# Performance work log

Hardware: AMD Instinct MI355X
Metric: run time of the kernel (lower is better)

Reference implementation:

```python
import jax, jax.numpy as jnp
import numpy as np

N = 2_000_000
C = 128
B = 50_000


def setup_inputs() -> dict:
    key = jax.random.key(0)
    k1, k2, k3 = jax.random.split(key, 3)
    x = jax.random.normal(k1, (N, C), dtype=jnp.float32)
    weight_c = jax.random.normal(k2, (C, C), dtype=jnp.float32) * (1.0 / np.sqrt(C))
    batch = jnp.sort(jax.random.randint(k3, (N,), 0, B, dtype=jnp.int64))
    return {"x": x, "weight_c": weight_c, "batch": batch, "num_segments": B}


def reference(x, weight_c, batch, num_segments):
    # global_mean_pool: segment sum / count (count clamped to >=1)
    sums = jax.ops.segment_sum(x, batch, num_segments=num_segments)          # [B, C]
    ones = jnp.ones((x.shape[0], 1), dtype=x.dtype)
    counts = jax.ops.segment_sum(ones, batch, num_segments=num_segments)    # [B, 1]
    c = sums / jnp.maximum(counts, 1.0)
    # context transform
    c = jnp.tanh(c @ weight_c)                                              # [B, C]
    # gather context back to nodes
    c_nodes = c[batch]                                                      # [N, C]
    # sigmoid gate on per-node dot product, then global_add_pool
    gate = jax.nn.sigmoid(jnp.sum(x * c_nodes, axis=1, keepdims=True))      # [N, 1]
    h = jax.ops.segment_sum(gate * x, batch, num_segments=num_segments)     # [B, C]
    return h
```

## Files before the change

### kernel.cpp

```cpp
#include <hip/hip_runtime.h>
#include <math.h>

#define C        128
#define BLK      256
#define WPB      (BLK / 64)
#define MAXSLOT  12
#define NROW     (4 * MAXSLOT)
#define WSTRIDE  68

__device__ __forceinline__ float4 f4add(float4 a, float4 b) {
    float4 r; r.x = a.x + b.x; r.y = a.y + b.y; r.z = a.z + b.z; r.w = a.w + b.w; return r;
}
__device__ __forceinline__ float4 f4shfl_xor(float4 v, int m) {
    float4 r;
    r.x = __shfl_xor(v.x, m, 64);
    r.y = __shfl_xor(v.y, m, 64);
    r.z = __shfl_xor(v.z, m, 64);
    r.w = __shfl_xor(v.w, m, 64);
    return r;
}
__device__ __forceinline__ float fast_tanh(float v) {
    const float t = __expf(2.0f * v);
    return 1.0f - 2.0f / (t + 1.0f);
}
__device__ __forceinline__ float fast_sigmoid(float v) {
    return 1.0f / (1.0f + __expf(-v));
}
__device__ __forceinline__ uint32_t pack2(float a, float b) {
    uint32_t ua = __float_as_uint(a), ub = __float_as_uint(b);
    ua = (ua + 0x7FFFu + ((ua >> 16) & 1u)) >> 16;
    ub = (ub + 0x7FFFu + ((ub >> 16) & 1u)) & 0xFFFF0000u;
    return ua | ub;
}
__device__ __forceinline__ float4 unpack4(uint32_t a, uint32_t b) {
    float4 v;
    v.x = __uint_as_float(a << 16);
    v.y = __uint_as_float(a & 0xFFFF0000u);
    v.z = __uint_as_float(b << 16);
    v.w = __uint_as_float(b & 0xFFFF0000u);
    return v;
}
__device__ __forceinline__ float row16_sum(float d) {
    d += __int_as_float(__builtin_amdgcn_update_dpp(0, __float_as_int(d), 0x128, 0xF, 0xF, true));
    d += __int_as_float(__builtin_amdgcn_update_dpp(0, __float_as_int(d), 0x124, 0xF, 0xF, true));
    d += __int_as_float(__builtin_amdgcn_update_dpp(0, __float_as_int(d), 0x122, 0xF, 0xF, true));
    d += __int_as_float(__builtin_amdgcn_update_dpp(0, __float_as_int(d), 0x121, 0xF, 0xF, true));
    return d;
}
__device__ __forceinline__ float dot8(float4 lo, float4 hi, float4 clo, float4 chi) {
    float a = lo.x * clo.x + lo.y * clo.y;
    float b = lo.z * clo.z + lo.w * clo.w;
    float c = hi.x * chi.x + hi.y * chi.y;
    float d = hi.z * chi.z + hi.w * chi.w;
    return (a + b) + (c + d);
}

extern "C" __global__ __launch_bounds__(BLK)
__attribute__((amdgpu_waves_per_eu(2, 2)))
void cba_pipe_reg_kernel(const float* __restrict__ x,
                         const float* __restrict__ W,
                         const int* __restrict__ batch,
                         float* __restrict__ out,
                         int N, int B, int totalWaves)
{
    __shared__ uint32_t sWb[C * WSTRIDE];
    __shared__ float4   sMean[WPB * 32];

    const int t    = threadIdx.x;
    const int lane = t & 63;
    const int wid  = t >> 6;
    const int rg   = lane >> 4;
    const int c16  = lane & 15;

    const float2* W2 = (const float2*)W;
    for (int p = t; p < C * 64; p += BLK) {
        const int k = p >> 6, j = p & 63;
        const float2 wv = W2[p];
        sWb[k * WSTRIDE + ((j + ((k >> 5) << 3)) & 63)] = pack2(wv.x, wv.y);
    }
    __syncthreads();

    const int gw = blockIdx.x * WPB + wid;

    const int qn = B / totalWaves;
    const int r  = B % totalWaves;
    const int segStart = gw * qn + (gw < r ? gw : r);
    const int myCnt    = qn + (gw < r ? 1 : 0);

    const int tl     = lane < myCnt ? lane : myCnt;
    const int target = segStart + tl;
    int lo_ = 0, hi_ = N;
    while (lo_ < hi_) {
        int mid = (lo_ + hi_) >> 1;
        if (batch[mid] < target) lo_ = mid + 1; else hi_ = mid;
    }
    const int bs = lo_;

    const float4* x4  = (const float4*)x;
    const int     Nm1 = N - 1;
    float4* mb = sMean + wid * 32;
    const int co = (((c16 << 2) + (rg << 3)) & 63);

    float4 pl[MAXSLOT], ph[MAXSLOT];

#define ISSUE(sseg)                                                    \
    {                                                                  \
        _Pragma("unroll")                                              \
        for (int sl = 0; sl < MAXSLOT; ++sl) {                         \
            const int row = (sseg) + 4 * sl + rg;                      \
            const int rc  = row < Nm1 ? row : Nm1;                     \
            pl[sl] = x4[(size_t)rc * 32 + (c16 << 1)];                 \
            ph[sl] = x4[(size_t)rc * 32 + (c16 << 1) + 1];             \
        }                                                              \
    }

    int sCur = 0, eCur = 0;
    if (myCnt > 0) {
        sCur = __shfl(bs, 0, 64);
        eCur = __shfl(bs, 1, 64);
        ISSUE(sCur);
    }

    for (int k = 0; k < myCnt; ++k) {
        const int b   = segStart + k;
        const int s   = sCur;
        const int e   = eCur;
        const int cnt = e - s;

        uint4 rbPk[MAXSLOT];
        float4 alo = make_float4(0.f,0.f,0.f,0.f), ahi = alo;
#pragma unroll
        for (int sl = 0; sl < MAXSLOT; ++sl) {
            const int  row   = s + 4 * sl + rg;
            const bool valid = row < e;
            float4 lo = pl[sl], hi = ph[sl];
            lo.x = valid ? lo.x : 0.f; lo.y = valid ? lo.y : 0.f;
            lo.z = valid ? lo.z : 0.f; lo.w = valid ? lo.w : 0.f;
            hi.x = valid ? hi.x : 0.f; hi.y = valid ? hi.y : 0.f;
            hi.z = valid ? hi.z : 0.f; hi.w = valid ? hi.w : 0.f;
            alo = f4add(alo, lo); ahi = f4add(ahi, hi);
            rbPk[sl].x = pack2(lo.x, lo.y); rbPk[sl].y = pack2(lo.z, lo.w);
            rbPk[sl].z = pack2(hi.x, hi.y); rbPk[sl].w = pack2(hi.z, hi.w);
        }
        for (int i = s + NROW + rg; i < e; i += 4) {
            alo = f4add(alo, x4[(size_t)i * 32 + (c16 << 1)]);
            ahi = f4add(ahi, x4[(size_t)i * 32 + (c16 << 1) + 1]);
        }

        if (k + 1 < myCnt) {
            sCur = __shfl(bs, k + 1, 64);
            eCur = __shfl(bs, k + 2, 64);
            ISSUE(sCur);
        }
        __builtin_amdgcn_sched_barrier(0);

        alo = f4add(alo, f4shfl_xor(alo, 16));
        alo = f4add(alo, f4shfl_xor(alo, 32));
        ahi = f4add(ahi, f4shfl_xor(ahi, 16));
        ahi = f4add(ahi, f4shfl_xor(ahi, 32));
        const float inv = 1.0f / (float)(cnt > 0 ? cnt : 1);
        if (lane < 16) {
            float4 mlo, mhi;
            mlo.x = alo.x*inv; mlo.y = alo.y*inv; mlo.z = alo.z*inv; mlo.w = alo.w*inv;
            mhi.x = ahi.x*inv; mhi.y = ahi.y*inv; mhi.z = ahi.z*inv; mhi.w = ahi.w*inv;
            mb[2 * c16]     = mlo;
            mb[2 * c16 + 1] = mhi;
        }

        float4 plo = make_float4(0.f,0.f,0.f,0.f), phi = plo;
#pragma unroll
        for (int jq = 0; jq < 8; ++jq) {
            const float4 m4 = mb[(rg << 3) + jq];
            const int kb = (rg << 5) + (jq << 2);
            const uint4 u0 = *(const uint4*)&sWb[(kb + 0) * WSTRIDE + co];
            const uint4 u1 = *(const uint4*)&sWb[(kb + 1) * WSTRIDE + co];
            const uint4 u2 = *(const uint4*)&sWb[(kb + 2) * WSTRIDE + co];
            const uint4 u3 = *(const uint4*)&sWb[(kb + 3) * WSTRIDE + co];
#define FMA8(mm, uu)                                                          \
            {                                                                 \
                plo.x = fmaf(mm, __uint_as_float((uu).x << 16),        plo.x);\
                plo.y = fmaf(mm, __uint_as_float((uu).x & 0xFFFF0000u),plo.y);\
                plo.z = fmaf(mm, __uint_as_float((uu).y << 16),        plo.z);\
                plo.w = fmaf(mm, __uint_as_float((uu).y & 0xFFFF0000u),plo.w);\
                phi.x = fmaf(mm, __uint_as_float((uu).z << 16),        phi.x);\
                phi.y = fmaf(mm, __uint_as_float((uu).z & 0xFFFF0000u),phi.y);\
                phi.z = fmaf(mm, __uint_as_float((uu).w << 16),        phi.z);\
                phi.w = fmaf(mm, __uint_as_float((uu).w & 0xFFFF0000u),phi.w);\
            }
            FMA8(m4.x, u0); FMA8(m4.y, u1); FMA8(m4.z, u2); FMA8(m4.w, u3);
#undef FMA8
        }
        plo = f4add(plo, f4shfl_xor(plo, 16));
        plo = f4add(plo, f4shfl_xor(plo, 32));
        phi = f4add(phi, f4shfl_xor(phi, 16));
        phi = f4add(phi, f4shfl_xor(phi, 32));
        float4 clo, chi;
        clo.x = fast_tanh(plo.x); clo.y = fast_tanh(plo.y);
        clo.z = fast_tanh(plo.z); clo.w = fast_tanh(plo.w);
        chi.x = fast_tanh(phi.x); chi.y = fast_tanh(phi.y);
        chi.z = fast_tanh(phi.z); chi.w = fast_tanh(phi.w);

        float4 hlo = make_float4(0.f,0.f,0.f,0.f), hhi = hlo;
#pragma unroll
        for (int sl = 0; sl < MAXSLOT; ++sl) {
            const float4 lo = unpack4(rbPk[sl].x, rbPk[sl].y);
            const float4 hi = unpack4(rbPk[sl].z, rbPk[sl].w);
            float d = dot8(lo, hi, clo, chi);
            d = row16_sum(d);
            const float g = fast_sigmoid(d);
            hlo.x = fmaf(g, lo.x, hlo.x); hlo.y = fmaf(g, lo.y, hlo.y);
            hlo.z = fmaf(g, lo.z, hlo.z); hlo.w = fmaf(g, lo.w, hlo.w);
            hhi.x = fmaf(g, hi.x, hhi.x); hhi.y = fmaf(g, hi.y, hhi.y);
            hhi.z = fmaf(g, hi.z, hhi.z); hhi.w = fmaf(g, hi.w, hhi.w);
        }
        for (int i = s + NROW + rg; i < e; i += 4) {
            const float4 lo = x4[(size_t)i * 32 + (c16 << 1)];
            const float4 hi = x4[(size_t)i * 32 + (c16 << 1) + 1];
            float d = dot8(lo, hi, clo, chi);
            d = row16_sum(d);
            const float g = fast_sigmoid(d);
            hlo.x = fmaf(g, lo.x, hlo.x); hlo.y = fmaf(g, lo.y, hlo.y);
            hlo.z = fmaf(g, lo.z, hlo.z); hlo.w = fmaf(g, lo.w, hlo.w);
            hhi.x = fmaf(g, hi.x, hhi.x); hhi.y = fmaf(g, hi.y, hhi.y);
            hhi.z = fmaf(g, hi.z, hhi.z); hhi.w = fmaf(g, hi.w, hhi.w);
        }
        hlo = f4add(hlo, f4shfl_xor(hlo, 16));
        hlo = f4add(hlo, f4shfl_xor(hlo, 32));
        hhi = f4add(hhi, f4shfl_xor(hhi, 16));
        hhi = f4add(hhi, f4shfl_xor(hhi, 32));
        if (lane < 16) {
            ((float4*)out)[(size_t)b * 32 + (c16 << 1)]     = hlo;
            ((float4*)out)[(size_t)b * 32 + (c16 << 1) + 1] = hhi;
        }
    }
#undef ISSUE
}

extern "C" void kernel_launch(void* const* d_in, const int* in_sizes, int n_in,
                              void* d_out, int out_size, void* d_ws, size_t ws_size,
                              hipStream_t stream) {
    const float* x     = (const float*)d_in[0];
    const float* W     = (const float*)d_in[1];
    const int*   batch = (const int*)d_in[2];
    float*       out   = (float*)d_out;

    const int N = in_sizes[0] / C;
    const int B = out_size / C;

    const int grid       = 512;
    const int totalWaves = grid * WPB;
    hipLaunchKernelGGL(cba_pipe_reg_kernel, dim3(grid), dim3(BLK), 0, stream,
                       x, W, batch, out, N, B, totalWaves);
}
```

Measured before the change: 269.5 us.

## Trade register-cached rows for three waves per EU and unrolled tail loops

Shrinks the per-segment register prefetch from 12 to 8 row slots so each wave needs fewer registers. That allows the occupancy hint to rise from 2 to 3 waves per EU, and the grid grows from 512 to 768 blocks to match. The overflow loops for segments longer than the cached window now handle two rows per iteration with a masked second load, giving more loads in flight. The cost is that more rows per segment (average about 40) fall outside the register cache and are read from global memory a second time in the gating pass.

New measurement: 289.9 us. 7.6% more time.

```diff
diff --git a/kernel.cpp b/kernel.cpp
--- a/kernel.cpp
+++ b/kernel.cpp
@@ -4,7 +4,7 @@
 #define C        128
 #define BLK      256
 #define WPB      (BLK / 64)
-#define MAXSLOT  12
+#define MAXSLOT  8
 #define NROW     (4 * MAXSLOT)
 #define WSTRIDE  68
 
@@ -19,6 +19,11 @@
     r.w = __shfl_xor(v.w, m, 64);
     return r;
 }
+__device__ __forceinline__ float4 f4mask(float4 v, bool keep) {
+    v.x = keep ? v.x : 0.f; v.y = keep ? v.y : 0.f;
+    v.z = keep ? v.z : 0.f; v.w = keep ? v.w : 0.f;
+    return v;
+}
 __device__ __forceinline__ float fast_tanh(float v) {
     const float t = __expf(2.0f * v);
     return 1.0f - 2.0f / (t + 1.0f);
@@ -56,12 +61,12 @@
 }
 
 extern "C" __global__ __launch_bounds__(BLK)
-__attribute__((amdgpu_waves_per_eu(2, 2)))
-void cba_pipe_reg_kernel(const float* __restrict__ x,
-                         const float* __restrict__ W,
-                         const int* __restrict__ batch,
-                         float* __restrict__ out,
-                         int N, int B, int totalWaves)
+__attribute__((amdgpu_waves_per_eu(3, 3)))
+void cba_pipe3_kernel(const float* __restrict__ x,
+                      const float* __restrict__ W,
+                      const int* __restrict__ batch,
+                      float* __restrict__ out,
+                      int N, int B, int totalWaves)
 {
     __shared__ uint32_t sWb[C * WSTRIDE];
     __shared__ float4   sMean[WPB * 32];
@@ -131,20 +136,23 @@
         float4 alo = make_float4(0.f,0.f,0.f,0.f), ahi = alo;
 #pragma unroll
         for (int sl = 0; sl < MAXSLOT; ++sl) {
-            const int  row   = s + 4 * sl + rg;
-            const bool valid = row < e;
-            float4 lo = pl[sl], hi = ph[sl];
-            lo.x = valid ? lo.x : 0.f; lo.y = valid ? lo.y : 0.f;
-            lo.z = valid ? lo.z : 0.f; lo.w = valid ? lo.w : 0.f;
-            hi.x = valid ? hi.x : 0.f; hi.y = valid ? hi.y : 0.f;
-            hi.z = valid ? hi.z : 0.f; hi.w = valid ? hi.w : 0.f;
+            const bool valid = (s + 4 * sl + rg) < e;
+            const float4 lo = f4mask(pl[sl], valid);
+            const float4 hi = f4mask(ph[sl], valid);
             alo = f4add(alo, lo); ahi = f4add(ahi, hi);
             rbPk[sl].x = pack2(lo.x, lo.y); rbPk[sl].y = pack2(lo.z, lo.w);
             rbPk[sl].z = pack2(hi.x, hi.y); rbPk[sl].w = pack2(hi.z, hi.w);
         }
-        for (int i = s + NROW + rg; i < e; i += 4) {
-            alo = f4add(alo, x4[(size_t)i * 32 + (c16 << 1)]);
-            ahi = f4add(ahi, x4[(size_t)i * 32 + (c16 << 1) + 1]);
+        for (int i = s + NROW + rg; i < e; i += 8) {
+            const int  i2 = i + 4;
+            const bool v2 = i2 < e;
+            const int  r2 = v2 ? i2 : i;
+            const float4 lo0 = x4[(size_t)i  * 32 + (c16 << 1)];
+            const float4 hi0 = x4[(size_t)i  * 32 + (c16 << 1) + 1];
+            const float4 lo1 = x4[(size_t)r2 * 32 + (c16 << 1)];
+            const float4 hi1 = x4[(size_t)r2 * 32 + (c16 << 1) + 1];
+            alo = f4add(alo, f4add(lo0, f4mask(lo1, v2)));
+            ahi = f4add(ahi, f4add(hi0, f4mask(hi1, v2)));
         }
 
         if (k + 1 < myCnt) {
@@ -213,16 +221,28 @@
             hhi.x = fmaf(g, hi.x, hhi.x); hhi.y = fmaf(g, hi.y, hhi.y);
             hhi.z = fmaf(g, hi.z, hhi.z); hhi.w = fmaf(g, hi.w, hhi.w);
         }
-        for (int i = s + NROW + rg; i < e; i += 4) {
-            const float4 lo = x4[(size_t)i * 32 + (c16 << 1)];
-            const float4 hi = x4[(size_t)i * 32 + (c16 << 1) + 1];
-            float d = dot8(lo, hi, clo, chi);
-            d = row16_sum(d);
-            const float g = fast_sigmoid(d);
-            hlo.x = fmaf(g, lo.x, hlo.x); hlo.y = fmaf(g, lo.y, hlo.y);
-            hlo.z = fmaf(g, lo.z, hlo.z); hlo.w = fmaf(g, lo.w, hlo.w);
-            hhi.x = fmaf(g, hi.x, hhi.x); hhi.y = fmaf(g, hi.y, hhi.y);
-            hhi.z = fmaf(g, hi.z, hhi.z); hhi.w = fmaf(g, hi.w, hhi.w);
+        for (int i = s + NROW + rg; i < e; i += 8) {
+            const int  i2 = i + 4;
+            const bool v2 = i2 < e;
+            const int  r2 = v2 ? i2 : i;
+            const float4 lo0 = x4[(size_t)i  * 32 + (c16 << 1)];
+            const float4 hi0 = x4[(size_t)i  * 32 + (c16 << 1) + 1];
+            float4 lo1 = f4mask(x4[(size_t)r2 * 32 + (c16 << 1)],     v2);
+            float4 hi1 = f4mask(x4[(size_t)r2 * 32 + (c16 << 1) + 1], v2);
+            float d0 = dot8(lo0, hi0, clo, chi);
+            float d1 = dot8(lo1, hi1, clo, chi);
+            d0 = row16_sum(d0);
+            d1 = row16_sum(d1);
+            const float g0 = fast_sigmoid(d0);
+            const float g1 = fast_sigmoid(d1);
+            hlo.x = fmaf(g0, lo0.x, hlo.x); hlo.y = fmaf(g0, lo0.y, hlo.y);
+            hlo.z = fmaf(g0, lo0.z, hlo.z); hlo.w = fmaf(g0, lo0.w, hlo.w);
+            hhi.x = fmaf(g0, hi0.x, hhi.x); hhi.y = fmaf(g0, hi0.y, hhi.y);
+            hhi.z = fmaf(g0, hi0.z, hhi.z); hhi.w = fmaf(g0, hi0.w, hhi.w);
+            hlo.x = fmaf(g1, lo1.x, hlo.x); hlo.y = fmaf(g1, lo1.y, hlo.y);
+            hlo.z = fmaf(g1, lo1.z, hlo.z); hlo.w = fmaf(g1, lo1.w, hlo.w);
+            hhi.x = fmaf(g1, hi1.x, hhi.x); hhi.y = fmaf(g1, hi1.y, hhi.y);
+            hhi.z = fmaf(g1, hi1.z, hhi.z); hhi.w = fmaf(g1, hi1.w, hhi.w);
         }
         hlo = f4add(hlo, f4shfl_xor(hlo, 16));
         hlo = f4add(hlo, f4shfl_xor(hlo, 32));
@@ -247,8 +267,8 @@
     const int N = in_sizes[0] / C;
     const int B = out_size / C;
 
-    const int grid       = 512;
+    const int grid       = 768;
     const int totalWaves = grid * WPB;
-    hipLaunchKernelGGL(cba_pipe_reg_kernel, dim3(grid), dim3(BLK), 0, stream,
+    hipLaunchKernelGGL(cba_pipe3_kernel, dim3(grid), dim3(BLK), 0, stream,
                        x, W, batch, out, N, B, totalWaves);
 }
```
